# Kernel tuning notes

Measured on AMD Instinct MI355X. Metric: run time of the kernel, lower is better.

The kernel has to match this reference:

```python
import jax, jax.numpy as jnp
import numpy as np

N = 30000        # nodes
E = 300000       # edges (before self-loops)
B = 300          # graphs
EMB = 64         # emb_dim (inner_dim overwritten to emb_dim in __init__)
HEADS = 4
OUT3 = 121       # hard-coded in conv3
H3 = 6           # heads of conv3
NCLS = 10
NVOC = 5000      # node token vocab for node_encoder
MAXD = 64        # max node depth for node_encoder


def _p(k, shape, scale=0.1):
    return scale * jax.random.normal(k, shape, dtype=jnp.float32)


def setup_inputs() -> dict:
    key = jax.random.key(0)
    ks = jax.random.split(key, 20)
    inp = {}
    inp["x"] = jax.random.randint(ks[0], (N, 1), 0, NVOC, dtype=jnp.int32)
    inp["node_depth"] = jax.random.randint(ks[1], (N, 1), 0, MAXD, dtype=jnp.int32)
    inp["edge_index"] = jax.random.randint(ks[2], (2, E), 0, N, dtype=jnp.int32)
    inp["batch"] = jnp.sort(jax.random.randint(ks[3], (N,), 0, B, dtype=jnp.int32))
    # node_encoder params (token emb + depth emb)
    inp["node_emb"] = _p(ks[4], (NVOC, EMB))
    inp["depth_emb"] = _p(ks[5], (MAXD, EMB))
    d1 = HEADS * EMB
    inp["w1"] = _p(ks[6], (EMB, d1))
    inp["as1"] = _p(ks[7], (HEADS, EMB))
    inp["ad1"] = _p(ks[8], (HEADS, EMB))
    inp["b1"] = jnp.zeros((d1,), jnp.float32)
    inp["w2"] = _p(ks[9], (d1, d1))
    inp["as2"] = _p(ks[10], (HEADS, EMB))
    inp["ad2"] = _p(ks[11], (HEADS, EMB))
    inp["b2"] = jnp.zeros((d1,), jnp.float32)
    d3 = H3 * OUT3
    inp["w3"] = _p(ks[12], (d1, d3))
    inp["as3"] = _p(ks[13], (H3, OUT3))
    inp["ad3"] = _p(ks[14], (H3, OUT3))
    inp["b3"] = jnp.zeros((d3,), jnp.float32)
    inp["wp"] = _p(ks[15], (OUT3, NCLS))
    inp["bp"] = jnp.zeros((NCLS,), jnp.float32)
    return inp


def gat_conv(x, W, a_src, a_dst, bias, src, dst, heads, out_dim):
    """PyG GATConv (concat=True, self-loops already in src/dst)."""
    n = x.shape[0]
    h = (x @ W).reshape(n, heads, out_dim)          # [N,H,D]
    es = (h * a_src).sum(-1)                        # [N,H] per-node src logits
    ed = (h * a_dst).sum(-1)                        # [N,H]
    e = jax.nn.leaky_relu(es[src] + ed[dst], 0.2)   # [E,H]
    # segment softmax over destination nodes (every node has a self-loop)
    m = jax.ops.segment_max(e, dst, num_segments=n)
    ex = jnp.exp(e - m[dst])
    s = jax.ops.segment_sum(ex, dst, num_segments=n)
    alpha = ex / (s[dst] + 1e-16)                   # [E,H]
    out = jax.ops.segment_sum(h[src] * alpha[:, :, None], dst, num_segments=n)
    return out.reshape(n, heads * out_dim) + bias


def reference(x, node_depth, edge_index, batch, node_emb, depth_emb,
              w1, as1, ad1, b1, w2, as2, ad2, b2, w3, as3, ad3, b3, wp, bp):
    n = x.shape[0]
    loops = jnp.arange(n, dtype=edge_index.dtype)
    src = jnp.concatenate([edge_index[0], loops])
    dst = jnp.concatenate([edge_index[1], loops])
    # node_encoder: token embedding + depth embedding
    h = node_emb[x[:, 0]] + depth_emb[node_depth.reshape(-1)]
    h = jax.nn.elu(gat_conv(h, w1, as1, ad1, b1, src, dst, HEADS, EMB))
    h = jax.nn.elu(gat_conv(h, w2, as2, ad2, b2, src, dst, HEADS, EMB))
    h = gat_conv(h, w3, as3, ad3, b3, src, dst, H3, OUT3)   # [N, 726]
    # global mean pool over graphs
    sums = jax.ops.segment_sum(h, batch, num_segments=B)
    cnt = jax.ops.segment_sum(jnp.ones((n,), h.dtype), batch, num_segments=B)
    g = sums / jnp.maximum(cnt, 1.0)[:, None]               # [B, 726]
    g = g.reshape(-1, H3, OUT3).mean(axis=1)                # [B, 121]
    return g @ wp + bp                                      # [B, NCLS]
```

## Files before the change

kernel.cpp:

```cpp
#include <hip/hip_runtime.h>
#include <hip/hip_bf16.h>
#include <math.h>

#define NN   30000
#define NE   300000
#define ETOT 330000
#define NB   300
#define EMB  64
#define D1   256
#define H1   4
#define H3   6
#define O3   121
#define D3   726
#define NQ   60
#define N3   72
#define NCLS 10
#define CAP  64

typedef __attribute__((ext_vector_type(8))) short short8;
typedef __attribute__((ext_vector_type(8))) unsigned short ushort8;
typedef __attribute__((ext_vector_type(4))) float floatx4;

static inline int ceil_div(int a, int b) { return (a + b - 1) / b; }

__device__ inline void split_bf16(float f, unsigned short& hi, unsigned short& lo) {
    __hip_bfloat16 h = __float2bfloat16(f);
    float fh = __bfloat162float(h);
    __hip_bfloat16 l = __float2bfloat16(f - fh);
    hi = __builtin_bit_cast(unsigned short, h);
    lo = __builtin_bit_cast(unsigned short, l);
}

__device__ inline float bf2f(unsigned short u) {
    return __builtin_bit_cast(float, (unsigned int)u << 16);
}

__device__ inline unsigned short f2bf(float f) {
    return __builtin_bit_cast(unsigned short, __float2bfloat16(f));
}

__device__ inline float lrelu(float v) { return v > 0.f ? v : 0.2f * v; }


__global__ void setup1_kernel(const int* __restrict__ x, const int* __restrict__ dep,
                              const float* __restrict__ nemb, const float* __restrict__ demb,
                              const float* __restrict__ w1,
                              unsigned short* __restrict__ H0hi, unsigned short* __restrict__ H0lo,
                              unsigned short* __restrict__ W1hi, unsigned short* __restrict__ W1lo,
                              int* __restrict__ cnt, float* __restrict__ G,
                              int* __restrict__ gs, int* __restrict__ ge) {
    int i = blockIdx.x * blockDim.x + threadIdx.x;
    if (i < NN * EMB) {
        int n = i >> 6, d = i & 63;
        float v = nemb[x[n] * EMB + d] + demb[dep[n] * EMB + d];
        split_bf16(v, H0hi[i], H0lo[i]);
    }
    if (i < NN) cnt[i] = 0;
    if (i < NB) { gs[i] = 0; ge[i] = 0; }
    if (i < NB * NCLS) G[i] = 0.f;
    if (i < EMB * D1) {
        int k = i / D1, n = i % D1;
        unsigned short h, l;
        split_bf16(w1[i], h, l);
        W1hi[n * EMB + k] = h;
        W1lo[n * EMB + k] = l;
    }
}


__global__ void setup2_kernel(const int* __restrict__ ei, const int* __restrict__ batch,
                              const float* __restrict__ w2, const float* __restrict__ w3,
                              const float* __restrict__ as3, const float* __restrict__ ad3,
                              const float* __restrict__ wp,
                              int* __restrict__ cnt, int* __restrict__ gs, int* __restrict__ ge,
                              unsigned short* __restrict__ W2b,
                              unsigned short* __restrict__ W3b,
                              int* __restrict__ csr) {
    int i = blockIdx.x * blockDim.x + threadIdx.x;
    if (i < ETOT) {
        int src, dst;
        if (i < NE) { src = ei[i]; dst = ei[NE + i]; }
        else        { src = i - NE; dst = src; }
        int slot = atomicAdd(&cnt[dst], 1);
        csr[dst * CAP + slot] = src;
    }
    if (i < NN) {
        int b = batch[i];
        if (i == 0 || batch[i - 1] != b) gs[b] = i;
        if (i == NN - 1 || batch[i + 1] != b) ge[b] = i + 1;
    }
    if (i < D1 * D1) {
        int k = i / D1, n = i % D1;
        W2b[n * D1 + k] = f2bf(w2[i]);
    }
    if (i < N3 * D1 * 8) {
        int oid = i >> 3, sub = i & 7;
        int n = oid / D1, k = oid % D1;
        const float* wrow = w3 + (size_t)k * D3;
        float acc = 0.f;
        if (n < NQ) {
            int h = n / NCLS, c = n % NCLS;
            const float* wr = wrow + h * O3;
            for (int j = sub; j < O3; j += 8) acc += wr[j] * wp[j * NCLS + c];
        } else if (n < NQ + H3) {
            int h = n - NQ;
            const float* wr = wrow + h * O3;
            for (int j = sub; j < O3; j += 8) acc += wr[j] * as3[h * O3 + j];
        } else {
            int h = n - NQ - H3;
            const float* wr = wrow + h * O3;
            for (int j = sub; j < O3; j += 8) acc += wr[j] * ad3[h * O3 + j];
        }
        acc += __shfl_xor(acc, 1);
        acc += __shfl_xor(acc, 2);
        acc += __shfl_xor(acc, 4);
        if (sub == 0) W3b[oid] = f2bf(acc);
    }
}


#define LDA 40

template <int MODE, bool SPLIT>
__global__ __launch_bounds__(256) void gemm_mfma_kernel(
    const unsigned short* __restrict__ Ahi, const unsigned short* __restrict__ Alo,
    const unsigned short* __restrict__ Bhi, const unsigned short* __restrict__ Blo,
    unsigned short* __restrict__ Cbf, unsigned short* __restrict__ Qb,
    float* __restrict__ es, float* __restrict__ ed,
    const float* __restrict__ as_, const float* __restrict__ ad_,
    int M, int K, int N) {
    __shared__ unsigned short sAh[128 * LDA], sBh[128 * LDA];
    __shared__ unsigned short sAl[SPLIT ? 128 * LDA : 1], sBl[SPLIT ? 128 * LDA : 1];
    int tid = threadIdx.x;
    int lane = tid & 63, wave = tid >> 6;
    int wr = (wave >> 1) * 64, wc = (wave & 1) * 64;
    int quad = lane >> 4, mr = lane & 15;
    int row0 = blockIdx.y * 128, col0 = blockIdx.x * 128;

    floatx4 zero = {0.f, 0.f, 0.f, 0.f};
    floatx4 acc[4][4];
    #pragma unroll
    for (int i = 0; i < 4; i++)
        #pragma unroll
        for (int j = 0; j < 4; j++) acc[i][j] = zero;

    for (int k0 = 0; k0 < K; k0 += 32) {
        #pragma unroll
        for (int ch = 0; ch < 2; ch++) {
            int linear = (ch * 256 + tid) * 8;
            int r = linear >> 5, c = linear & 31;
            uint4 vh, vl;
            int gr = row0 + r;
            if (gr < M) {
                vh = *(const uint4*)(Ahi + (size_t)gr * K + k0 + c);
                if (SPLIT) vl = *(const uint4*)(Alo + (size_t)gr * K + k0 + c);
            } else { vh = uint4{0, 0, 0, 0}; vl = uint4{0, 0, 0, 0}; }
            *(uint4*)&sAh[r * LDA + c] = vh;
            if (SPLIT) *(uint4*)&sAl[r * LDA + c] = vl;
            int gn = col0 + r;
            if (gn < N) {
                vh = *(const uint4*)(Bhi + (size_t)gn * K + k0 + c);
                if (SPLIT) vl = *(const uint4*)(Blo + (size_t)gn * K + k0 + c);
            } else { vh = uint4{0, 0, 0, 0}; vl = uint4{0, 0, 0, 0}; }
            *(uint4*)&sBh[r * LDA + c] = vh;
            if (SPLIT) *(uint4*)&sBl[r * LDA + c] = vl;
        }
        __syncthreads();

        short8 ah[4], al[4], bh[4], bl[4];
        #pragma unroll
        for (int i = 0; i < 4; i++) {
            int ar = wr + i * 16 + mr;
            ah[i] = *(const short8*)&sAh[ar * LDA + quad * 8];
            if (SPLIT) al[i] = *(const short8*)&sAl[ar * LDA + quad * 8];
            int br = wc + i * 16 + mr;
            bh[i] = *(const short8*)&sBh[br * LDA + quad * 8];
            if (SPLIT) bl[i] = *(const short8*)&sBl[br * LDA + quad * 8];
        }
        #pragma unroll
        for (int i = 0; i < 4; i++)
            #pragma unroll
            for (int j = 0; j < 4; j++) {
                acc[i][j] = __builtin_amdgcn_mfma_f32_16x16x32_bf16(ah[i], bh[j], acc[i][j], 0, 0, 0);
                if (SPLIT) {
                    acc[i][j] = __builtin_amdgcn_mfma_f32_16x16x32_bf16(ah[i], bl[j], acc[i][j], 0, 0, 0);
                    acc[i][j] = __builtin_amdgcn_mfma_f32_16x16x32_bf16(al[i], bh[j], acc[i][j], 0, 0, 0);
                }
            }
        __syncthreads();
    }

    #pragma unroll
    for (int i = 0; i < 4; i++) {
        #pragma unroll
        for (int j = 0; j < 4; j++) {
            int gc = col0 + wc + j * 16 + mr;
            if (gc >= N) continue;
            int gr0 = row0 + wr + i * 16 + quad * 4;
            #pragma unroll
            for (int r = 0; r < 4; r++) {
                int gr = gr0 + r;
                if (gr >= M) continue;
                float v = acc[i][j][r];
                if (MODE == 0) {
                    Cbf[(size_t)gr * D1 + gc] = f2bf(v);
                } else {
                    if (gc < NQ)            Qb[(size_t)gr * NQ + gc] = f2bf(v);
                    else if (gc < NQ + H3)  es[(size_t)gr * H3 + (gc - NQ)] = v;
                    else                    ed[(size_t)gr * H3 + (gc - NQ - H3)] = v;
                }
            }
        }
    }

    if (MODE == 0) {
        int hx = 2 * blockIdx.x + (wave & 1);
        float asr[4], adr[4];
        #pragma unroll
        for (int j = 0; j < 4; j++) {
            asr[j] = as_[hx * 64 + j * 16 + mr];
            adr[j] = ad_[hx * 64 + j * 16 + mr];
        }
        #pragma unroll
        for (int i = 0; i < 4; i++) {
            #pragma unroll
            for (int r = 0; r < 4; r++) {
                float ps = 0.f, pd = 0.f;
                #pragma unroll
                for (int j = 0; j < 4; j++) {
                    float v = acc[i][j][r];
                    ps += v * asr[j];
                    pd += v * adr[j];
                }
                #pragma unroll
                for (int m2 = 8; m2 >= 1; m2 >>= 1) {
                    ps += __shfl_xor(ps, m2);
                    pd += __shfl_xor(pd, m2);
                }
                int gr = row0 + wr + i * 16 + quad * 4 + r;
                if (mr == 0 && gr < M) {
                    es[gr * 4 + hx] = ps;
                    ed[gr * 4 + hx] = pd;
                }
            }
        }
    }
}


__global__ __launch_bounds__(256) void aggregate12_kernel(
    const unsigned short* __restrict__ P, const float* __restrict__ es,
    const float* __restrict__ ed, const int* __restrict__ cnt,
    const int* __restrict__ csr, const float* __restrict__ bias,
    unsigned short* __restrict__ outHi) {
    int wave = threadIdx.x >> 6, lane = threadIdx.x & 63;
    int wid = blockIdx.x * 4 + wave;
    int hi = lane >> 5;
    int fl = lane & 31;
    int hq = fl >> 3;
    int f0 = fl * 8;
    float bv[8];
    #pragma unroll
    for (int j = 0; j < 8; j++) bv[j] = bias[f0 + j];
    #pragma unroll 1
    for (int t = 0; t < 4; t++) {
        int dst = wid * 4 + t;
        int s0 = dst * CAP, s1 = s0 + cnt[dst];
        float edv = ed[dst * 4 + hq];
        float sum = 0.f;
        float acc[8];
        #pragma unroll
        for (int j = 0; j < 8; j++) acc[j] = 0.f;
        int s = s0;
        for (; s + 8 <= s1; s += 8) {
            int si[4]; float ev[4]; ushort8 pp[4];
            #pragma unroll
            for (int u = 0; u < 4; u++) si[u] = csr[s + 2 * u + hi];
            #pragma unroll
            for (int u = 0; u < 4; u++) {
                ev[u] = es[si[u] * 4 + hq] + edv;
                pp[u] = *(const ushort8*)(P + (size_t)si[u] * D1 + f0);
            }
            #pragma unroll
            for (int u = 0; u < 4; u++) {
                float e = __expf(lrelu(ev[u]));
                sum += e;
                #pragma unroll
                for (int j = 0; j < 8; j++) acc[j] += e * bf2f(pp[u][j]);
            }
        }
        for (; s + 4 <= s1; s += 4) {
            int si[2]; float ev[2]; ushort8 pp[2];
            #pragma unroll
            for (int u = 0; u < 2; u++) si[u] = csr[s + 2 * u + hi];
            #pragma unroll
            for (int u = 0; u < 2; u++) {
                ev[u] = es[si[u] * 4 + hq] + edv;
                pp[u] = *(const ushort8*)(P + (size_t)si[u] * D1 + f0);
            }
            #pragma unroll
            for (int u = 0; u < 2; u++) {
                float e = __expf(lrelu(ev[u]));
                sum += e;
                #pragma unroll
                for (int j = 0; j < 8; j++) acc[j] += e * bf2f(pp[u][j]);
            }
        }
        for (; s < s1; s += 2) {
            int idx = s + hi;
            bool v = idx < s1;
            int si = csr[v ? idx : s];
            float evv = es[si * 4 + hq] + edv;
            ushort8 p8 = *(const ushort8*)(P + (size_t)si * D1 + f0);
            float e = v ? __expf(lrelu(evv)) : 0.f;
            sum += e;
            #pragma unroll
            for (int j = 0; j < 8; j++) acc[j] += e * bf2f(p8[j]);
        }
        sum += __shfl_xor(sum, 32);
        #pragma unroll
        for (int j = 0; j < 8; j++) acc[j] += __shfl_xor(acc[j], 32);
        float inv = 1.f / sum;
        if (lane < 32) {
            ushort8 o8;
            #pragma unroll
            for (int j = 0; j < 8; j++) {
                float a = acc[j] * inv + bv[j];
                a = a > 0.f ? a : expm1f(a);
                o8[j] = f2bf(a);
            }
            *(ushort8*)(outHi + (size_t)dst * D1 + f0) = o8;
        }
    }
}


__global__ __launch_bounds__(256) void aggregate3q_kernel(
    const unsigned short* __restrict__ Qb, const float* __restrict__ es,
    const float* __restrict__ ed, const int* __restrict__ cnt,
    const int* __restrict__ csr, const int* __restrict__ batch,
    float* __restrict__ G) {
    int wave = threadIdx.x >> 6, lane = threadIdx.x & 63;
    int wid = blockIdx.x * 4 + wave;
    bool act = lane < NQ;
    int h = act ? (lane / NCLS) : 0;
    int q = act ? lane : 0;
    #pragma unroll 1
    for (int t = 0; t < 4; t++) {
        int dst = wid * 4 + t;
        int b = batch[dst];
        int s0 = dst * CAP, s1 = s0 + cnt[dst];
        float edv = act ? ed[dst * H3 + h] : 0.f;
        float sum = 0.f, acc = 0.f;
        int s = s0;
        for (; s + 8 <= s1; s += 8) {
            int si[8];
            #pragma unroll
            for (int u = 0; u < 8; u++) si[u] = csr[s + u];
            float vv[8], qq[8];
            #pragma unroll
            for (int u = 0; u < 8; u++) {
                vv[u] = es[si[u] * H3 + h] + edv;
                qq[u] = bf2f(Qb[(size_t)si[u] * NQ + q]);
            }
            #pragma unroll
            for (int u = 0; u < 8; u++) {
                float e = __expf(lrelu(vv[u]));
                sum += e;
                acc += e * qq[u];
            }
        }
        for (; s + 2 <= s1; s += 2) {
            int sa = csr[s], sb = csr[s + 1];
            float va = es[sa * H3 + h] + edv;
            float vb = es[sb * H3 + h] + edv;
            float qa = bf2f(Qb[(size_t)sa * NQ + q]);
            float qb = bf2f(Qb[(size_t)sb * NQ + q]);
            float ea = __expf(lrelu(va));
            float eb = __expf(lrelu(vb));
            sum += ea + eb;
            acc += ea * qa + eb * qb;
        }
        for (; s < s1; s++) {
            int sa = csr[s];
            float va = es[sa * H3 + h] + edv;
            float qa = bf2f(Qb[(size_t)sa * NQ + q]);
            float ea = __expf(lrelu(va));
            sum += ea;
            acc += ea * qa;
        }
        acc *= 1.f / sum;
        float av = act ? acc : 0.f;
        float tot = av;
        #pragma unroll
        for (int h2 = 1; h2 < H3; h2++) tot += __shfl(av, lane + h2 * NCLS);
        if (lane < NCLS) atomicAdd(&G[b * NCLS + lane], tot);
    }
}


__global__ __launch_bounds__(64) void final_kernel(
    const float* __restrict__ G, const int* __restrict__ gs, const int* __restrict__ ge,
    const float* __restrict__ b3, const float* __restrict__ wp,
    const float* __restrict__ bp, float* __restrict__ out) {
    int b = blockIdx.x, tid = threadIdx.x;
    if (tid >= NCLS) return;
    int cntn = ge[b] - gs[b];
    float o = bp[tid];
    if (cntn > 0) {
        float bt = 0.f;
        for (int k = 0; k < O3; k++) {
            float bs = 0.f;
            #pragma unroll
            for (int h = 0; h < H3; h++) bs += b3[h * O3 + k];
            bt += bs * wp[k * NCLS + tid];
        }
        o += G[b * NCLS + tid] / (6.f * (float)cntn) + bt * (1.f / 6.f);
    }
    out[b * NCLS + tid] = o;
}


extern "C" void kernel_launch(void* const* d_in, const int* in_sizes, int n_in,
                              void* d_out, int out_size, void* d_ws, size_t ws_size,
                              hipStream_t stream) {
    const int* x     = (const int*)d_in[0];
    const int* dep   = (const int*)d_in[1];
    const int* ei    = (const int*)d_in[2];
    const int* batch = (const int*)d_in[3];
    const float* nemb = (const float*)d_in[4];
    const float* demb = (const float*)d_in[5];
    const float* w1  = (const float*)d_in[6];
    const float* as1 = (const float*)d_in[7];
    const float* ad1 = (const float*)d_in[8];
    const float* b1  = (const float*)d_in[9];
    const float* w2  = (const float*)d_in[10];
    const float* as2 = (const float*)d_in[11];
    const float* ad2 = (const float*)d_in[12];
    const float* b2  = (const float*)d_in[13];
    const float* w3  = (const float*)d_in[14];
    const float* as3 = (const float*)d_in[15];
    const float* ad3 = (const float*)d_in[16];
    const float* b3  = (const float*)d_in[17];
    const float* wp  = (const float*)d_in[18];
    const float* bp  = (const float*)d_in[19];
    float* out = (float*)d_out;

    char* ws = (char*)d_ws;
    size_t off = 0;
    auto alloc = [&](size_t bytes) -> void* {
        void* p = ws + off;
        off += (bytes + 255) & ~(size_t)255;
        return p;
    };
    unsigned short* Hb   = (unsigned short*)alloc((size_t)NN * D1 * 2);
    unsigned short* H0lo = (unsigned short*)alloc((size_t)NN * EMB * 2);
    unsigned short* W1hi = (unsigned short*)alloc((size_t)D1 * EMB * 2);
    unsigned short* W1lo = (unsigned short*)alloc((size_t)D1 * EMB * 2);
    unsigned short* W2b  = (unsigned short*)alloc((size_t)D1 * D1 * 2);
    unsigned short* W3b  = (unsigned short*)alloc((size_t)N3 * D1 * 2);
    unsigned short* Pb   = (unsigned short*)alloc((size_t)NN * D1 * 2);
    unsigned short* Qb   = (unsigned short*)alloc(((size_t)NN * NQ + 64) * 2);
    float* G    = (float*)alloc((size_t)NB * NCLS * 4);
    float* es   = (float*)alloc((size_t)NN * 6 * 4);
    float* ed   = (float*)alloc((size_t)NN * 6 * 4);
    int* cnt    = (int*)alloc((size_t)NN * 4);
    int* csr    = (int*)alloc((size_t)NN * CAP * 4);
    int* gs     = (int*)alloc((size_t)NB * 4);
    int* ge     = (int*)alloc((size_t)NB * 4);

    setup1_kernel<<<ceil_div(NN * EMB, 256), 256, 0, stream>>>(
        x, dep, nemb, demb, w1, Hb, H0lo, W1hi, W1lo, cnt, G, gs, ge);
    setup2_kernel<<<ceil_div(ETOT, 256), 256, 0, stream>>>(
        ei, batch, w2, w3, as3, ad3, wp, cnt, gs, ge, W2b, W3b, csr);

    gemm_mfma_kernel<0, true><<<dim3(2, ceil_div(NN, 128)), 256, 0, stream>>>(
        Hb, H0lo, W1hi, W1lo, Pb, nullptr, es, ed, as1, ad1, NN, EMB, D1);
    aggregate12_kernel<<<NN / 16, 256, 0, stream>>>(Pb, es, ed, cnt, csr, b1, Hb);

    gemm_mfma_kernel<0, false><<<dim3(2, ceil_div(NN, 128)), 256, 0, stream>>>(
        Hb, nullptr, W2b, nullptr, Pb, nullptr, es, ed, as2, ad2, NN, D1, D1);
    aggregate12_kernel<<<NN / 16, 256, 0, stream>>>(Pb, es, ed, cnt, csr, b2, Hb);

    gemm_mfma_kernel<1, false><<<dim3(1, ceil_div(NN, 128)), 256, 0, stream>>>(
        Hb, nullptr, W3b, nullptr, nullptr, Qb, es, ed, nullptr, nullptr, NN, D1, N3);
    aggregate3q_kernel<<<NN / 16, 256, 0, stream>>>(Qb, es, ed, cnt, csr, batch, G);

    final_kernel<<<NB, 64, 0, stream>>>(G, gs, ge, b3, wp, bp, out);
}
```

Before: 270.9 us.

## Fuse all GAT stages into one cooperative persistent kernel with grid syncs

Replaces the sequence of eight kernel launches (setup, three GEMMs, three aggregations, final pool) with a single cooperative persistent kernel whose phases are separated by grid-wide barriers. Work in each phase is distributed with grid-stride or tile-stride loops, and the grid size is set from CU count times occupancy. The goal is to remove per-launch overhead and inter-kernel gaps. In exchange the grid is limited to resident blocks (at most 1024), shared memory is sized for the largest phase, and every phase transition costs a grid sync. A multi-kernel fallback runs if the cooperative launch fails.

```diff
diff --git a/kernel.cpp b/kernel.cpp
--- a/kernel.cpp
+++ b/kernel.cpp
@@ -1,6 +1,9 @@
 #include <hip/hip_runtime.h>
+#include <hip/hip_cooperative_groups.h>
 #include <hip/hip_bf16.h>
 #include <math.h>
+
+namespace cg = cooperative_groups;
 
 #define NN   30000
 #define NE   300000
@@ -16,6 +19,7 @@
 #define N3   72
 #define NCLS 10
 #define CAP  64
+#define LDA  40
 
 typedef __attribute__((ext_vector_type(8))) short short8;
 typedef __attribute__((ext_vector_type(8))) unsigned short ushort8;
@@ -42,219 +46,225 @@
 __device__ inline float lrelu(float v) { return v > 0.f ? v : 0.2f * v; }
 
 
-__global__ void setup1_kernel(const int* __restrict__ x, const int* __restrict__ dep,
-                              const float* __restrict__ nemb, const float* __restrict__ demb,
-                              const float* __restrict__ w1,
-                              unsigned short* __restrict__ H0hi, unsigned short* __restrict__ H0lo,
-                              unsigned short* __restrict__ W1hi, unsigned short* __restrict__ W1lo,
-                              int* __restrict__ cnt, float* __restrict__ G,
-                              int* __restrict__ gs, int* __restrict__ ge) {
-    int i = blockIdx.x * blockDim.x + threadIdx.x;
-    if (i < NN * EMB) {
-        int n = i >> 6, d = i & 63;
-        float v = nemb[x[n] * EMB + d] + demb[dep[n] * EMB + d];
-        split_bf16(v, H0hi[i], H0lo[i]);
-    }
-    if (i < NN) cnt[i] = 0;
-    if (i < NB) { gs[i] = 0; ge[i] = 0; }
-    if (i < NB * NCLS) G[i] = 0.f;
-    if (i < EMB * D1) {
-        int k = i / D1, n = i % D1;
-        unsigned short h, l;
-        split_bf16(w1[i], h, l);
-        W1hi[n * EMB + k] = h;
-        W1lo[n * EMB + k] = l;
-    }
-}
-
-
-__global__ void setup2_kernel(const int* __restrict__ ei, const int* __restrict__ batch,
-                              const float* __restrict__ w2, const float* __restrict__ w3,
-                              const float* __restrict__ as3, const float* __restrict__ ad3,
-                              const float* __restrict__ wp,
-                              int* __restrict__ cnt, int* __restrict__ gs, int* __restrict__ ge,
-                              unsigned short* __restrict__ W2b,
-                              unsigned short* __restrict__ W3b,
-                              int* __restrict__ csr) {
-    int i = blockIdx.x * blockDim.x + threadIdx.x;
-    if (i < ETOT) {
-        int src, dst;
-        if (i < NE) { src = ei[i]; dst = ei[NE + i]; }
-        else        { src = i - NE; dst = src; }
-        int slot = atomicAdd(&cnt[dst], 1);
-        csr[dst * CAP + slot] = src;
-    }
-    if (i < NN) {
-        int b = batch[i];
-        if (i == 0 || batch[i - 1] != b) gs[b] = i;
-        if (i == NN - 1 || batch[i + 1] != b) ge[b] = i + 1;
-    }
-    if (i < D1 * D1) {
-        int k = i / D1, n = i % D1;
-        W2b[n * D1 + k] = f2bf(w2[i]);
-    }
-    if (i < N3 * D1 * 8) {
-        int oid = i >> 3, sub = i & 7;
-        int n = oid / D1, k = oid % D1;
-        const float* wrow = w3 + (size_t)k * D3;
-        float acc = 0.f;
-        if (n < NQ) {
-            int h = n / NCLS, c = n % NCLS;
-            const float* wr = wrow + h * O3;
-            for (int j = sub; j < O3; j += 8) acc += wr[j] * wp[j * NCLS + c];
-        } else if (n < NQ + H3) {
-            int h = n - NQ;
-            const float* wr = wrow + h * O3;
-            for (int j = sub; j < O3; j += 8) acc += wr[j] * as3[h * O3 + j];
-        } else {
-            int h = n - NQ - H3;
-            const float* wr = wrow + h * O3;
-            for (int j = sub; j < O3; j += 8) acc += wr[j] * ad3[h * O3 + j];
-        }
-        acc += __shfl_xor(acc, 1);
-        acc += __shfl_xor(acc, 2);
-        acc += __shfl_xor(acc, 4);
-        if (sub == 0) W3b[oid] = f2bf(acc);
-    }
-}
-
-
-#define LDA 40
+__device__ __forceinline__ void phase_zero(int* __restrict__ cnt, float* __restrict__ G,
+                                           int* __restrict__ gs, int* __restrict__ ge) {
+    int base = blockIdx.x * blockDim.x + threadIdx.x;
+    int stride = gridDim.x * blockDim.x;
+    const int TOT = NN + NB * NCLS + 2 * NB;
+    for (int i = base; i < TOT; i += stride) {
+        if (i < NN) cnt[i] = 0;
+        else if (i < NN + NB * NCLS) G[i - NN] = 0.f;
+        else if (i < NN + NB * NCLS + NB) gs[i - NN - NB * NCLS] = 0;
+        else ge[i - NN - NB * NCLS - NB] = 0;
+    }
+}
+
+__device__ __forceinline__ void phase_setup(
+    const int* __restrict__ x, const int* __restrict__ dep,
+    const int* __restrict__ ei, const int* __restrict__ batch,
+    const float* __restrict__ nemb, const float* __restrict__ demb,
+    const float* __restrict__ w1, const float* __restrict__ w2,
+    const float* __restrict__ w3, const float* __restrict__ as3,
+    const float* __restrict__ ad3, const float* __restrict__ wp,
+    unsigned short* __restrict__ H0hi, unsigned short* __restrict__ H0lo,
+    unsigned short* __restrict__ W1hi, unsigned short* __restrict__ W1lo,
+    unsigned short* __restrict__ W2b, unsigned short* __restrict__ W3b,
+    int* __restrict__ cnt, int* __restrict__ csr,
+    int* __restrict__ gs, int* __restrict__ ge) {
+    int base = blockIdx.x * blockDim.x + threadIdx.x;
+    int stride = gridDim.x * blockDim.x;
+    for (int i = base; i < NN * EMB; i += stride) {
+        {
+            int n = i >> 6, d = i & 63;
+            float v = nemb[x[n] * EMB + d] + demb[dep[n] * EMB + d];
+            split_bf16(v, H0hi[i], H0lo[i]);
+        }
+        if (i < ETOT) {
+            int src, dst;
+            if (i < NE) { src = ei[i]; dst = ei[NE + i]; }
+            else        { src = i - NE; dst = src; }
+            int slot = atomicAdd(&cnt[dst], 1);
+            csr[dst * CAP + slot] = src;
+        }
+        if (i < NN) {
+            int b = batch[i];
+            if (i == 0 || batch[i - 1] != b) gs[b] = i;
+            if (i == NN - 1 || batch[i + 1] != b) ge[b] = i + 1;
+        }
+        if (i < EMB * D1) {
+            int k = i / D1, n = i % D1;
+            unsigned short h, l;
+            split_bf16(w1[i], h, l);
+            W1hi[n * EMB + k] = h;
+            W1lo[n * EMB + k] = l;
+        }
+        if (i < D1 * D1) {
+            int k = i / D1, n = i % D1;
+            W2b[n * D1 + k] = f2bf(w2[i]);
+        }
+        if (i < N3 * D1 * 8) {
+            int oid = i >> 3, sub = i & 7;
+            int n = oid / D1, k = oid % D1;
+            const float* wrow = w3 + (size_t)k * D3;
+            float acc = 0.f;
+            if (n < NQ) {
+                int h = n / NCLS, c = n % NCLS;
+                const float* wr = wrow + h * O3;
+                for (int j = sub; j < O3; j += 8) acc += wr[j] * wp[j * NCLS + c];
+            } else if (n < NQ + H3) {
+                int h = n - NQ;
+                const float* wr = wrow + h * O3;
+                for (int j = sub; j < O3; j += 8) acc += wr[j] * as3[h * O3 + j];
+            } else {
+                int h = n - NQ - H3;
+                const float* wr = wrow + h * O3;
+                for (int j = sub; j < O3; j += 8) acc += wr[j] * ad3[h * O3 + j];
+            }
+            acc += __shfl_xor(acc, 1);
+            acc += __shfl_xor(acc, 2);
+            acc += __shfl_xor(acc, 4);
+            if (sub == 0) W3b[oid] = f2bf(acc);
+        }
+    }
+}
 
 template <int MODE, bool SPLIT>
-__global__ __launch_bounds__(256) void gemm_mfma_kernel(
+__device__ __forceinline__ void gemm_phase(
+    unsigned short* __restrict__ sAh, unsigned short* __restrict__ sAl,
+    unsigned short* __restrict__ sBh, unsigned short* __restrict__ sBl,
     const unsigned short* __restrict__ Ahi, const unsigned short* __restrict__ Alo,
     const unsigned short* __restrict__ Bhi, const unsigned short* __restrict__ Blo,
     unsigned short* __restrict__ Cbf, unsigned short* __restrict__ Qb,
     float* __restrict__ es, float* __restrict__ ed,
     const float* __restrict__ as_, const float* __restrict__ ad_,
-    int M, int K, int N) {
-    __shared__ unsigned short sAh[128 * LDA], sBh[128 * LDA];
-    __shared__ unsigned short sAl[SPLIT ? 128 * LDA : 1], sBl[SPLIT ? 128 * LDA : 1];
+    int M, int K, int N, int nbx) {
     int tid = threadIdx.x;
     int lane = tid & 63, wave = tid >> 6;
     int wr = (wave >> 1) * 64, wc = (wave & 1) * 64;
     int quad = lane >> 4, mr = lane & 15;
-    int row0 = blockIdx.y * 128, col0 = blockIdx.x * 128;
-
-    floatx4 zero = {0.f, 0.f, 0.f, 0.f};
-    floatx4 acc[4][4];
-    #pragma unroll
-    for (int i = 0; i < 4; i++)
+    int nby = (M + 127) >> 7;
+    int ntiles = nbx * nby;
+
+    for (int tile = blockIdx.x; tile < ntiles; tile += gridDim.x) {
+        int row0 = (tile / nbx) * 128, col0 = (tile % nbx) * 128;
+
+        floatx4 zero = {0.f, 0.f, 0.f, 0.f};
+        floatx4 acc[4][4];
         #pragma unroll
-        for (int j = 0; j < 4; j++) acc[i][j] = zero;
-
-    for (int k0 = 0; k0 < K; k0 += 32) {
-        #pragma unroll
-        for (int ch = 0; ch < 2; ch++) {
-            int linear = (ch * 256 + tid) * 8;
-            int r = linear >> 5, c = linear & 31;
-            uint4 vh, vl;
-            int gr = row0 + r;
-            if (gr < M) {
-                vh = *(const uint4*)(Ahi + (size_t)gr * K + k0 + c);
-                if (SPLIT) vl = *(const uint4*)(Alo + (size_t)gr * K + k0 + c);
-            } else { vh = uint4{0, 0, 0, 0}; vl = uint4{0, 0, 0, 0}; }
-            *(uint4*)&sAh[r * LDA + c] = vh;
-            if (SPLIT) *(uint4*)&sAl[r * LDA + c] = vl;
-            int gn = col0 + r;
-            if (gn < N) {
-                vh = *(const uint4*)(Bhi + (size_t)gn * K + k0 + c);
-                if (SPLIT) vl = *(const uint4*)(Blo + (size_t)gn * K + k0 + c);
-            } else { vh = uint4{0, 0, 0, 0}; vl = uint4{0, 0, 0, 0}; }
-            *(uint4*)&sBh[r * LDA + c] = vh;
-            if (SPLIT) *(uint4*)&sBl[r * LDA + c] = vl;
-        }
-        __syncthreads();
-
-        short8 ah[4], al[4], bh[4], bl[4];
+        for (int i = 0; i < 4; i++)
+            #pragma unroll
+            for (int j = 0; j < 4; j++) acc[i][j] = zero;
+
+        for (int k0 = 0; k0 < K; k0 += 32) {
+            #pragma unroll
+            for (int ch = 0; ch < 2; ch++) {
+                int linear = (ch * 256 + tid) * 8;
+                int r = linear >> 5, c = linear & 31;
+                uint4 vh, vl;
+                int gr = row0 + r;
+                if (gr < M) {
+                    vh = *(const uint4*)(Ahi + (size_t)gr * K + k0 + c);
+                    if (SPLIT) vl = *(const uint4*)(Alo + (size_t)gr * K + k0 + c);
+                } else { vh = uint4{0, 0, 0, 0}; vl = uint4{0, 0, 0, 0}; }
+                *(uint4*)&sAh[r * LDA + c] = vh;
+                if (SPLIT) *(uint4*)&sAl[r * LDA + c] = vl;
+                int gn = col0 + r;
+                if (gn < N) {
+                    vh = *(const uint4*)(Bhi + (size_t)gn * K + k0 + c);
+                    if (SPLIT) vl = *(const uint4*)(Blo + (size_t)gn * K + k0 + c);
+                } else { vh = uint4{0, 0, 0, 0}; vl = uint4{0, 0, 0, 0}; }
+                *(uint4*)&sBh[r * LDA + c] = vh;
+                if (SPLIT) *(uint4*)&sBl[r * LDA + c] = vl;
+            }
+            __syncthreads();
+
+            short8 ah[4], al[4], bh[4], bl[4];
+            #pragma unroll
+            for (int i = 0; i < 4; i++) {
+                int ar = wr + i * 16 + mr;
+                ah[i] = *(const short8*)&sAh[ar * LDA + quad * 8];
+                if (SPLIT) al[i] = *(const short8*)&sAl[ar * LDA + quad * 8];
+                int br = wc + i * 16 + mr;
+                bh[i] = *(const short8*)&sBh[br * LDA + quad * 8];
+                if (SPLIT) bl[i] = *(const short8*)&sBl[br * LDA + quad * 8];
+            }
+            #pragma unroll
+            for (int i = 0; i < 4; i++)
+                #pragma unroll
+                for (int j = 0; j < 4; j++) {
+                    acc[i][j] = __builtin_amdgcn_mfma_f32_16x16x32_bf16(ah[i], bh[j], acc[i][j], 0, 0, 0);
+                    if (SPLIT) {
+                        acc[i][j] = __builtin_amdgcn_mfma_f32_16x16x32_bf16(ah[i], bl[j], acc[i][j], 0, 0, 0);
+                        acc[i][j] = __builtin_amdgcn_mfma_f32_16x16x32_bf16(al[i], bh[j], acc[i][j], 0, 0, 0);
+                    }
+                }
+            __syncthreads();
+        }
+
         #pragma unroll
         for (int i = 0; i < 4; i++) {
-            int ar = wr + i * 16 + mr;
-            ah[i] = *(const short8*)&sAh[ar * LDA + quad * 8];
-            if (SPLIT) al[i] = *(const short8*)&sAl[ar * LDA + quad * 8];
-            int br = wc + i * 16 + mr;
-            bh[i] = *(const short8*)&sBh[br * LDA + quad * 8];
-            if (SPLIT) bl[i] = *(const short8*)&sBl[br * LDA + quad * 8];
-        }
-        #pragma unroll
-        for (int i = 0; i < 4; i++)
             #pragma unroll
             for (int j = 0; j < 4; j++) {
-                acc[i][j] = __builtin_amdgcn_mfma_f32_16x16x32_bf16(ah[i], bh[j], acc[i][j], 0, 0, 0);
-                if (SPLIT) {
-                    acc[i][j] = __builtin_amdgcn_mfma_f32_16x16x32_bf16(ah[i], bl[j], acc[i][j], 0, 0, 0);
-                    acc[i][j] = __builtin_amdgcn_mfma_f32_16x16x32_bf16(al[i], bh[j], acc[i][j], 0, 0, 0);
+                int gc = col0 + wc + j * 16 + mr;
+                if (gc >= N) continue;
+                int gr0 = row0 + wr + i * 16 + quad * 4;
+                #pragma unroll
+                for (int r = 0; r < 4; r++) {
+                    int gr = gr0 + r;
+                    if (gr >= M) continue;
+                    float v = acc[i][j][r];
+                    if (MODE == 0) {
+                        Cbf[(size_t)gr * D1 + gc] = f2bf(v);
+                    } else {
+                        if (gc < NQ)            Qb[(size_t)gr * NQ + gc] = f2bf(v);
+                        else if (gc < NQ + H3)  es[(size_t)gr * H3 + (gc - NQ)] = v;
+                        else                    ed[(size_t)gr * H3 + (gc - NQ - H3)] = v;
+                    }
                 }
             }
-        __syncthreads();
-    }
-
-    #pragma unroll
-    for (int i = 0; i < 4; i++) {
-        #pragma unroll
-        for (int j = 0; j < 4; j++) {
-            int gc = col0 + wc + j * 16 + mr;
-            if (gc >= N) continue;
-            int gr0 = row0 + wr + i * 16 + quad * 4;
-            #pragma unroll
-            for (int r = 0; r < 4; r++) {
-                int gr = gr0 + r;
-                if (gr >= M) continue;
-                float v = acc[i][j][r];
-                if (MODE == 0) {
-                    Cbf[(size_t)gr * D1 + gc] = f2bf(v);
-                } else {
-                    if (gc < NQ)            Qb[(size_t)gr * NQ + gc] = f2bf(v);
-                    else if (gc < NQ + H3)  es[(size_t)gr * H3 + (gc - NQ)] = v;
-                    else                    ed[(size_t)gr * H3 + (gc - NQ - H3)] = v;
+        }
+
+        if (MODE == 0) {
+            int hx = 2 * (tile % nbx) + (wave & 1);
+            float asr[4], adr[4];
+            #pragma unroll
+            for (int j = 0; j < 4; j++) {
+                asr[j] = as_[hx * 64 + j * 16 + mr];
+                adr[j] = ad_[hx * 64 + j * 16 + mr];
+            }
+            #pragma unroll
+            for (int i = 0; i < 4; i++) {
+                #pragma unroll
+                for (int r = 0; r < 4; r++) {
+                    float ps = 0.f, pd = 0.f;
+                    #pragma unroll
+                    for (int j = 0; j < 4; j++) {
+                        float v = acc[i][j][r];
+                        ps += v * asr[j];
+                        pd += v * adr[j];
+                    }
+                    #pragma unroll
+                    for (int m2 = 8; m2 >= 1; m2 >>= 1) {
+                        ps += __shfl_xor(ps, m2);
+                        pd += __shfl_xor(pd, m2);
+                    }
+                    int gr = row0 + wr + i * 16 + quad * 4 + r;
+                    if (mr == 0 && gr < M) {
+                        es[gr * 4 + hx] = ps;
+                        ed[gr * 4 + hx] = pd;
+                    }
                 }
             }
         }
     }
-
-    if (MODE == 0) {
-        int hx = 2 * blockIdx.x + (wave & 1);
-        float asr[4], adr[4];
-        #pragma unroll
-        for (int j = 0; j < 4; j++) {
-            asr[j] = as_[hx * 64 + j * 16 + mr];
-            adr[j] = ad_[hx * 64 + j * 16 + mr];
-        }
-        #pragma unroll
-        for (int i = 0; i < 4; i++) {
-            #pragma unroll
-            for (int r = 0; r < 4; r++) {
-                float ps = 0.f, pd = 0.f;
-                #pragma unroll
-                for (int j = 0; j < 4; j++) {
-                    float v = acc[i][j][r];
-                    ps += v * asr[j];
-                    pd += v * adr[j];
-                }
-                #pragma unroll
-                for (int m2 = 8; m2 >= 1; m2 >>= 1) {
-                    ps += __shfl_xor(ps, m2);
-                    pd += __shfl_xor(pd, m2);
-                }
-                int gr = row0 + wr + i * 16 + quad * 4 + r;
-                if (mr == 0 && gr < M) {
-                    es[gr * 4 + hx] = ps;
-                    ed[gr * 4 + hx] = pd;
-                }
-            }
-        }
-    }
-}
-
-
-__global__ __launch_bounds__(256) void aggregate12_kernel(
+}
+
+__device__ __forceinline__ void agg12_phase(
     const unsigned short* __restrict__ P, const float* __restrict__ es,
     const float* __restrict__ ed, const int* __restrict__ cnt,
     const int* __restrict__ csr, const float* __restrict__ bias,
     unsigned short* __restrict__ outHi) {
     int wave = threadIdx.x >> 6, lane = threadIdx.x & 63;
-    int wid = blockIdx.x * 4 + wave;
     int hi = lane >> 5;
     int fl = lane & 31;
     int hq = fl >> 3;
@@ -262,9 +272,7 @@
     float bv[8];
     #pragma unroll
     for (int j = 0; j < 8; j++) bv[j] = bias[f0 + j];
-    #pragma unroll 1
-    for (int t = 0; t < 4; t++) {
-        int dst = wid * 4 + t;
+    for (int dst = blockIdx.x * 4 + wave; dst < NN; dst += gridDim.x * 4) {
         int s0 = dst * CAP, s1 = s0 + cnt[dst];
         float edv = ed[dst * 4 + hq];
         float sum = 0.f;
@@ -334,20 +342,16 @@
     }
 }
 
-
-__global__ __launch_bounds__(256) void aggregate3q_kernel(
+__device__ __forceinline__ void agg3q_phase(
     const unsigned short* __restrict__ Qb, const float* __restrict__ es,
     const float* __restrict__ ed, const int* __restrict__ cnt,
     const int* __restrict__ csr, const int* __restrict__ batch,
     float* __restrict__ G) {
     int wave = threadIdx.x >> 6, lane = threadIdx.x & 63;
-    int wid = blockIdx.x * 4 + wave;
     bool act = lane < NQ;
     int h = act ? (lane / NCLS) : 0;
     int q = act ? lane : 0;
-    #pragma unroll 1
-    for (int t = 0; t < 4; t++) {
-        int dst = wid * 4 + t;
+    for (int dst = blockIdx.x * 4 + wave; dst < NN; dst += gridDim.x * 4) {
         int b = batch[dst];
         int s0 = dst * CAP, s1 = s0 + cnt[dst];
         float edv = act ? ed[dst * H3 + h] : 0.f;
@@ -398,53 +402,151 @@
     }
 }
 
-
-__global__ __launch_bounds__(64) void final_kernel(
+__device__ __forceinline__ void final_phase(
     const float* __restrict__ G, const int* __restrict__ gs, const int* __restrict__ ge,
     const float* __restrict__ b3, const float* __restrict__ wp,
     const float* __restrict__ bp, float* __restrict__ out) {
-    int b = blockIdx.x, tid = threadIdx.x;
-    if (tid >= NCLS) return;
-    int cntn = ge[b] - gs[b];
-    float o = bp[tid];
-    if (cntn > 0) {
-        float bt = 0.f;
-        for (int k = 0; k < O3; k++) {
-            float bs = 0.f;
-            #pragma unroll
-            for (int h = 0; h < H3; h++) bs += b3[h * O3 + k];
-            bt += bs * wp[k * NCLS + tid];
-        }
-        o += G[b * NCLS + tid] / (6.f * (float)cntn) + bt * (1.f / 6.f);
-    }
-    out[b * NCLS + tid] = o;
+    int wave = threadIdx.x >> 6, lane = threadIdx.x & 63;
+    for (int b = blockIdx.x * 4 + wave; b < NB; b += gridDim.x * 4) {
+        if (lane < NCLS) {
+            int cntn = ge[b] - gs[b];
+            float o = bp[lane];
+            if (cntn > 0) {
+                float bt = 0.f;
+                for (int k = 0; k < O3; k++) {
+                    float bs = 0.f;
+                    #pragma unroll
+                    for (int hh = 0; hh < H3; hh++) bs += b3[hh * O3 + k];
+                    bt += bs * wp[k * NCLS + lane];
+                }
+                o += G[b * NCLS + lane] / (6.f * (float)cntn) + bt * (1.f / 6.f);
+            }
+            out[b * NCLS + lane] = o;
+        }
+    }
+}
+
+
+struct MegaArgs {
+    const int *x, *dep, *ei, *batch;
+    const float *nemb, *demb, *w1, *as1, *ad1, *b1, *w2, *as2, *ad2, *b2;
+    const float *w3, *as3, *ad3, *b3, *wp, *bp;
+    float* out;
+    unsigned short *Hb, *H0lo, *W1hi, *W1lo, *W2b, *W3b, *Pb, *Qb;
+    float *G, *es, *ed;
+    int *cnt, *csr, *gs, *ge;
+};
+
+__global__ __launch_bounds__(256, 2) void mega_kernel(MegaArgs a) {
+    __shared__ unsigned short sAh[128 * LDA], sBh[128 * LDA];
+    __shared__ unsigned short sAl[128 * LDA], sBl[128 * LDA];
+    cg::grid_group grid = cg::this_grid();
+
+    phase_zero(a.cnt, a.G, a.gs, a.ge);
+    grid.sync();
+
+    phase_setup(a.x, a.dep, a.ei, a.batch, a.nemb, a.demb, a.w1, a.w2, a.w3,
+                a.as3, a.ad3, a.wp, a.Hb, a.H0lo, a.W1hi, a.W1lo, a.W2b, a.W3b,
+                a.cnt, a.csr, a.gs, a.ge);
+    grid.sync();
+
+    gemm_phase<0, true>(sAh, sAl, sBh, sBl, a.Hb, a.H0lo, a.W1hi, a.W1lo,
+                        a.Pb, nullptr, a.es, a.ed, a.as1, a.ad1, NN, EMB, D1, 2);
+    grid.sync();
+
+    agg12_phase(a.Pb, a.es, a.ed, a.cnt, a.csr, a.b1, a.Hb);
+    grid.sync();
+
+    gemm_phase<0, false>(sAh, sAl, sBh, sBl, a.Hb, nullptr, a.W2b, nullptr,
+                         a.Pb, nullptr, a.es, a.ed, a.as2, a.ad2, NN, D1, D1, 2);
+    grid.sync();
+
+    agg12_phase(a.Pb, a.es, a.ed, a.cnt, a.csr, a.b2, a.Hb);
+    grid.sync();
+
+    gemm_phase<1, false>(sAh, sAl, sBh, sBl, a.Hb, nullptr, a.W3b, nullptr,
+                         nullptr, a.Qb, a.es, a.ed, nullptr, nullptr, NN, D1, N3, 1);
+    grid.sync();
+
+    agg3q_phase(a.Qb, a.es, a.ed, a.cnt, a.csr, a.batch, a.G);
+    grid.sync();
+
+    final_phase(a.G, a.gs, a.ge, a.b3, a.wp, a.bp, a.out);
+}
+
+
+__global__ void fb_zero_kernel(int* cnt, float* G, int* gs, int* ge) {
+    phase_zero(cnt, G, gs, ge);
+}
+
+__global__ void fb_setup_kernel(const int* x, const int* dep, const int* ei, const int* batch,
+                                const float* nemb, const float* demb, const float* w1,
+                                const float* w2, const float* w3, const float* as3,
+                                const float* ad3, const float* wp,
+                                unsigned short* H0hi, unsigned short* H0lo,
+                                unsigned short* W1hi, unsigned short* W1lo,
+                                unsigned short* W2b, unsigned short* W3b,
+                                int* cnt, int* csr, int* gs, int* ge) {
+    phase_setup(x, dep, ei, batch, nemb, demb, w1, w2, w3, as3, ad3, wp,
+                H0hi, H0lo, W1hi, W1lo, W2b, W3b, cnt, csr, gs, ge);
+}
+
+template <int MODE, bool SPLIT>
+__global__ __launch_bounds__(256) void fb_gemm_kernel(
+    const unsigned short* Ahi, const unsigned short* Alo,
+    const unsigned short* Bhi, const unsigned short* Blo,
+    unsigned short* Cbf, unsigned short* Qb, float* es, float* ed,
+    const float* as_, const float* ad_, int M, int K, int N, int nbx) {
+    __shared__ unsigned short sAh[128 * LDA], sBh[128 * LDA];
+    __shared__ unsigned short sAl[SPLIT ? 128 * LDA : 1], sBl[SPLIT ? 128 * LDA : 1];
+    gemm_phase<MODE, SPLIT>(sAh, sAl, sBh, sBl, Ahi, Alo, Bhi, Blo,
+                            Cbf, Qb, es, ed, as_, ad_, M, K, N, nbx);
+}
+
+__global__ __launch_bounds__(256) void fb_agg12_kernel(
+    const unsigned short* P, const float* es, const float* ed, const int* cnt,
+    const int* csr, const float* bias, unsigned short* outHi) {
+    agg12_phase(P, es, ed, cnt, csr, bias, outHi);
+}
+
+__global__ __launch_bounds__(256) void fb_agg3q_kernel(
+    const unsigned short* Qb, const float* es, const float* ed, const int* cnt,
+    const int* csr, const int* batch, float* G) {
+    agg3q_phase(Qb, es, ed, cnt, csr, batch, G);
+}
+
+__global__ __launch_bounds__(256) void fb_final_kernel(
+    const float* G, const int* gs, const int* ge, const float* b3,
+    const float* wp, const float* bp, float* out) {
+    final_phase(G, gs, ge, b3, wp, bp, out);
 }
 
 
 extern "C" void kernel_launch(void* const* d_in, const int* in_sizes, int n_in,
                               void* d_out, int out_size, void* d_ws, size_t ws_size,
                               hipStream_t stream) {
-    const int* x     = (const int*)d_in[0];
-    const int* dep   = (const int*)d_in[1];
-    const int* ei    = (const int*)d_in[2];
-    const int* batch = (const int*)d_in[3];
-    const float* nemb = (const float*)d_in[4];
-    const float* demb = (const float*)d_in[5];
-    const float* w1  = (const float*)d_in[6];
-    const float* as1 = (const float*)d_in[7];
-    const float* ad1 = (const float*)d_in[8];
-    const float* b1  = (const float*)d_in[9];
-    const float* w2  = (const float*)d_in[10];
-    const float* as2 = (const float*)d_in[11];
-    const float* ad2 = (const float*)d_in[12];
-    const float* b2  = (const float*)d_in[13];
-    const float* w3  = (const float*)d_in[14];
-    const float* as3 = (const float*)d_in[15];
-    const float* ad3 = (const float*)d_in[16];
-    const float* b3  = (const float*)d_in[17];
-    const float* wp  = (const float*)d_in[18];
-    const float* bp  = (const float*)d_in[19];
-    float* out = (float*)d_out;
+    MegaArgs a;
+    a.x     = (const int*)d_in[0];
+    a.dep   = (const int*)d_in[1];
+    a.ei    = (const int*)d_in[2];
+    a.batch = (const int*)d_in[3];
+    a.nemb  = (const float*)d_in[4];
+    a.demb  = (const float*)d_in[5];
+    a.w1    = (const float*)d_in[6];
+    a.as1   = (const float*)d_in[7];
+    a.ad1   = (const float*)d_in[8];
+    a.b1    = (const float*)d_in[9];
+    a.w2    = (const float*)d_in[10];
+    a.as2   = (const float*)d_in[11];
+    a.ad2   = (const float*)d_in[12];
+    a.b2    = (const float*)d_in[13];
+    a.w3    = (const float*)d_in[14];
+    a.as3   = (const float*)d_in[15];
+    a.ad3   = (const float*)d_in[16];
+    a.b3    = (const float*)d_in[17];
+    a.wp    = (const float*)d_in[18];
+    a.bp    = (const float*)d_in[19];
+    a.out   = (float*)d_out;
 
     char* ws = (char*)d_ws;
     size_t off = 0;
@@ -453,38 +555,58 @@
         off += (bytes + 255) & ~(size_t)255;
         return p;
     };
-    unsigned short* Hb   = (unsigned short*)alloc((size_t)NN * D1 * 2);
-    unsigned short* H0lo = (unsigned short*)alloc((size_t)NN * EMB * 2);
-    unsigned short* W1hi = (unsigned short*)alloc((size_t)D1 * EMB * 2);
-    unsigned short* W1lo = (unsigned short*)alloc((size_t)D1 * EMB * 2);
-    unsigned short* W2b  = (unsigned short*)alloc((size_t)D1 * D1 * 2);
-    unsigned short* W3b  = (unsigned short*)alloc((size_t)N3 * D1 * 2);
-    unsigned short* Pb   = (unsigned short*)alloc((size_t)NN * D1 * 2);
-    unsigned short* Qb   = (unsigned short*)alloc(((size_t)NN * NQ + 64) * 2);
-    float* G    = (float*)alloc((size_t)NB * NCLS * 4);
-    float* es   = (float*)alloc((size_t)NN * 6 * 4);
-    float* ed   = (float*)alloc((size_t)NN * 6 * 4);
-    int* cnt    = (int*)alloc((size_t)NN * 4);
-    int* csr    = (int*)alloc((size_t)NN * CAP * 4);
-    int* gs     = (int*)alloc((size_t)NB * 4);
-    int* ge     = (int*)alloc((size_t)NB * 4);
-
-    setup1_kernel<<<ceil_div(NN * EMB, 256), 256, 0, stream>>>(
-        x, dep, nemb, demb, w1, Hb, H0lo, W1hi, W1lo, cnt, G, gs, ge);
-    setup2_kernel<<<ceil_div(ETOT, 256), 256, 0, stream>>>(
-        ei, batch, w2, w3, as3, ad3, wp, cnt, gs, ge, W2b, W3b, csr);
-
-    gemm_mfma_kernel<0, true><<<dim3(2, ceil_div(NN, 128)), 256, 0, stream>>>(
-        Hb, H0lo, W1hi, W1lo, Pb, nullptr, es, ed, as1, ad1, NN, EMB, D1);
-    aggregate12_kernel<<<NN / 16, 256, 0, stream>>>(Pb, es, ed, cnt, csr, b1, Hb);
-
-    gemm_mfma_kernel<0, false><<<dim3(2, ceil_div(NN, 128)), 256, 0, stream>>>(
-        Hb, nullptr, W2b, nullptr, Pb, nullptr, es, ed, as2, ad2, NN, D1, D1);
-    aggregate12_kernel<<<NN / 16, 256, 0, stream>>>(Pb, es, ed, cnt, csr, b2, Hb);
-
-    gemm_mfma_kernel<1, false><<<dim3(1, ceil_div(NN, 128)), 256, 0, stream>>>(
-        Hb, nullptr, W3b, nullptr, nullptr, Qb, es, ed, nullptr, nullptr, NN, D1, N3);
-    aggregate3q_kernel<<<NN / 16, 256, 0, stream>>>(Qb, es, ed, cnt, csr, batch, G);
-
-    final_kernel<<<NB, 64, 0, stream>>>(G, gs, ge, b3, wp, bp, out);
-}
+    a.Hb   = (unsigned short*)alloc((size_t)NN * D1 * 2);
+    a.H0lo = (unsigned short*)alloc((size_t)NN * EMB * 2);
+    a.W1hi = (unsigned short*)alloc((size_t)D1 * EMB * 2);
+    a.W1lo = (unsigned short*)alloc((size_t)D1 * EMB * 2);
+    a.W2b  = (unsigned short*)alloc((size_t)D1 * D1 * 2);
+    a.W3b  = (unsigned short*)alloc((size_t)N3 * D1 * 2);
+    a.Pb   = (unsigned short*)alloc((size_t)NN * D1 * 2);
+    a.Qb   = (unsigned short*)alloc(((size_t)NN * NQ + 64) * 2);
+    a.G    = (float*)alloc((size_t)NB * NCLS * 4);
+    a.es   = (float*)alloc((size_t)NN * 6 * 4);
+    a.ed   = (float*)alloc((size_t)NN * 6 * 4);
+    a.cnt  = (int*)alloc((size_t)NN * 4);
+    a.csr  = (int*)alloc((size_t)NN * CAP * 4);
+    a.gs   = (int*)alloc((size_t)NB * 4);
+    a.ge   = (int*)alloc((size_t)NB * 4);
+
+    static int s_grid = 0;
+    if (s_grid == 0) {
+        int dev = 0;
+        (void)hipGetDevice(&dev);
+        int cus = 0;
+        if (hipDeviceGetAttribute(&cus, hipDeviceAttributeMultiprocessorCount, dev) != hipSuccess || cus <= 0)
+            cus = 256;
+        int occ = 0;
+        if (hipOccupancyMaxActiveBlocksPerMultiprocessor(&occ, (const void*)mega_kernel, 256, 0) != hipSuccess || occ <= 0)
+            occ = 2;
+        long long g = (long long)cus * occ;
+        if (g > 1024) g = 1024;
+        s_grid = (int)g;
+    }
+
+    void* kargs[] = { (void*)&a };
+    hipError_t e = hipLaunchCooperativeKernel((const void*)mega_kernel,
+                                              dim3(s_grid), dim3(256), kargs, 0, stream);
+    if (e != hipSuccess) {
+        fb_zero_kernel<<<ceil_div(NN + NB * NCLS + 2 * NB, 256), 256, 0, stream>>>(
+            a.cnt, a.G, a.gs, a.ge);
+        fb_setup_kernel<<<ceil_div(NN * EMB, 256), 256, 0, stream>>>(
+            a.x, a.dep, a.ei, a.batch, a.nemb, a.demb, a.w1, a.w2, a.w3, a.as3, a.ad3, a.wp,
+            a.Hb, a.H0lo, a.W1hi, a.W1lo, a.W2b, a.W3b, a.cnt, a.csr, a.gs, a.ge);
+        fb_gemm_kernel<0, true><<<2 * ceil_div(NN, 128), 256, 0, stream>>>(
+            a.Hb, a.H0lo, a.W1hi, a.W1lo, a.Pb, nullptr, a.es, a.ed, a.as1, a.ad1,
+            NN, EMB, D1, 2);
+        fb_agg12_kernel<<<NN / 16, 256, 0, stream>>>(a.Pb, a.es, a.ed, a.cnt, a.csr, a.b1, a.Hb);
+        fb_gemm_kernel<0, false><<<2 * ceil_div(NN, 128), 256, 0, stream>>>(
+            a.Hb, nullptr, a.W2b, nullptr, a.Pb, nullptr, a.es, a.ed, a.as2, a.ad2,
+            NN, D1, D1, 2);
+        fb_agg12_kernel<<<NN / 16, 256, 0, stream>>>(a.Pb, a.es, a.ed, a.cnt, a.csr, a.b2, a.Hb);
+        fb_gemm_kernel<1, false><<<ceil_div(NN, 128), 256, 0, stream>>>(
+            a.Hb, nullptr, a.W3b, nullptr, nullptr, a.Qb, a.es, a.ed, nullptr, nullptr,
+            NN, D1, N3, 1);
+        fb_agg3q_kernel<<<NN / 16, 256, 0, stream>>>(a.Qb, a.es, a.ed, a.cnt, a.csr, a.batch, a.G);
+        fb_final_kernel<<<ceil_div(NB, 4), 256, 0, stream>>>(a.G, a.gs, a.ge, a.b3, a.wp, a.bp, a.out);
+    }
+}
```

Measured after the change: 691.5 us. 155% more time.
